# Kernel optimization log

Hardware: AMD Instinct MI355X
Metric: run time of the kernel (lower is better)

Reference implementation:

```python
import jax, jax.numpy as jnp
import numpy as np

B, S, D = 4, 2048, 1024
H = 16
HD = D // H  # 64


def setup_inputs() -> dict:
    key = jax.random.key(0)
    ks = jax.random.split(key, 5)
    std = 1.0 / np.sqrt(D)
    return {
        "x": jax.random.normal(ks[0], (B, S, D), dtype=jnp.float32),
        "Wq": jax.random.normal(ks[1], (D, D), dtype=jnp.float32) * std,
        "Wk": jax.random.normal(ks[2], (D, D), dtype=jnp.float32) * std,
        "Wv": jax.random.normal(ks[3], (D, D), dtype=jnp.float32) * std,
        "Wo": jax.random.normal(ks[4], (D, D), dtype=jnp.float32) * std,
        "bo": jnp.zeros((D,), dtype=jnp.float32),
    }


def reference(x, Wq, Wk, Wv, Wo, bo):
    b, n, d_in = x.shape
    q = (x @ Wq).reshape(b, n, H, HD).transpose(0, 2, 1, 3)  # [b,h,n,hd]
    k = (x @ Wk).reshape(b, n, H, HD).transpose(0, 2, 1, 3)
    v = (x @ Wv).reshape(b, n, H, HD).transpose(0, 2, 1, 3)
    scores = jnp.einsum("bhqd,bhkd->bhqk", q, k)  # full NxN, as in original
    causal = jnp.tril(jnp.ones((n, n), dtype=bool))  # True = keep
    scores = jnp.where(causal, scores, -jnp.inf)
    attn = jax.nn.softmax(scores / np.sqrt(HD), axis=-1)
    # dropout p=0.0 -> identity
    ctx = jnp.einsum("bhqk,bhkd->bqhd", attn, v).reshape(b, n, H * HD)
    return ctx @ Wo + bo
```

## Files before the change

### kernel.cpp

```cpp
#include <hip/hip_runtime.h>
#include <math.h>

#define BATCH 4
#define SLEN 2048
#define DMODEL 1024
#define NH 16
#define HD 64
#define MROWS (BATCH * SLEN)
#define QK_LD 2048

typedef __attribute__((ext_vector_type(8))) short short8;
typedef __attribute__((ext_vector_type(4))) float floatx4;

#define AS1 __attribute__((address_space(1)))
#define AS3 __attribute__((address_space(3)))

__device__ inline unsigned short f2bf(float f) {
    union { float f; unsigned u; } a; a.f = f;
    unsigned r = a.u + 0x7fff + ((a.u >> 16) & 1);
    return (unsigned short)(r >> 16);
}

__device__ inline unsigned pack_bf(float lo, float hi) {
    union { float f; unsigned u; } a, b; a.f = lo; b.f = hi;
    return __builtin_amdgcn_perm(b.u + 0x8000u, a.u + 0x8000u, 0x07060302u);
}
__device__ inline unsigned pack_tr(float lo, float hi) {
    union { float f; unsigned u; } a, b; a.f = lo; b.f = hi;
    return __builtin_amdgcn_perm(b.u, a.u, 0x07060302u);
}

__global__ __launch_bounds__(256) void cvt_all(
    const float* __restrict__ x,
    const float* __restrict__ Wq, const float* __restrict__ Wk,
    const float* __restrict__ Wv, const float* __restrict__ Wo,
    short* __restrict__ xb,
    short* __restrict__ WqkT, short* __restrict__ WvT, short* __restrict__ WoT)
{
    int bid = blockIdx.x;
    if (bid < 8192) {
        int i = (bid * 256 + threadIdx.x) * 4;
        float4 v = *(const float4*)(x + i);
        unsigned short t0 = f2bf(v.x), t1 = f2bf(v.y), t2 = f2bf(v.z), t3 = f2bf(v.w);
        uint2 o;
        o.x = (unsigned)t0 | ((unsigned)t1 << 16);
        o.y = (unsigned)t2 | ((unsigned)t3 << 16);
        *(uint2*)(xb + i) = o;
    } else {
        bid -= 8192;
        int z = bid >> 10;
        int inner = bid & 1023;
        int bxi = inner & 31, byi = inner >> 5;

        const float* W; short* Wt; float sc = 1.0f;
        if (z == 0)      { W = Wq; Wt = WqkT; sc = 0.18033688011112042f; }
        else if (z == 1) { W = Wk; Wt = WqkT + (size_t)DMODEL * DMODEL; }
        else if (z == 2) { W = Wv; Wt = WvT; }
        else             { W = Wo; Wt = WoT; }

        __shared__ float t[32][33];
        int bn = bxi * 32, bk = byi * 32;
        int tx = threadIdx.x & 31, r0 = (threadIdx.x >> 5) * 4;
        #pragma unroll
        for (int i = 0; i < 4; i++)
            t[r0 + i][tx] = W[(size_t)(bk + r0 + i) * DMODEL + bn + tx];
        __syncthreads();
        #pragma unroll
        for (int i = 0; i < 4; i++)
            Wt[(size_t)(bn + r0 + i) * DMODEL + bk + tx] = (short)f2bf(t[tx][r0 + i] * sc);
    }
}

#define TM 128
#define TN 128
#define TK 32

template <int OUT_BF16>
__device__ __forceinline__ void gemm_body(
    const short* __restrict__ A,
    const short* __restrict__ Bt,
    const float* __restrict__ bias,
    void* __restrict__ Cout, int N, int K, int m0, int n0)
{
    __shared__ short As[2][TM * TK];
    __shared__ short Bs[2][TN * TK];
    int tid = threadIdx.x;
    int l = tid & 63, w = tid >> 6;
    int wm = (w >> 1) * 64, wn = (w & 1) * 64;
    int lr = l & 15, lk = (l >> 4) * 8;

    const short* asrc[2];
    const short* bsrc[2];
    #pragma unroll
    for (int r = 0; r < 2; r++) {
        int c = r * 256 + tid;
        int mm = c >> 2, kk = (c & 3) * 8;
        asrc[r] = A  + (size_t)(m0 + mm) * K + kk;
        bsrc[r] = Bt + (size_t)(n0 + mm) * K + kk;
    }

    floatx4 acc[4][4] = {};

    #pragma unroll
    for (int r = 0; r < 2; r++) {
        int c = r * 256 + tid;
        __builtin_amdgcn_global_load_lds((const AS1 void*)asrc[r],
            (AS3 void*)(&As[0][0] + c * 8), 16, 0, 0);
        __builtin_amdgcn_global_load_lds((const AS1 void*)bsrc[r],
            (AS3 void*)(&Bs[0][0] + c * 8), 16, 0, 0);
        asrc[r] += TK; bsrc[r] += TK;
    }

    int nk = K / TK;
    for (int t = 0; t < nk; t++) {
        int cur = t & 1;
        if (t + 1 < nk) {
            #pragma unroll
            for (int r = 0; r < 2; r++) {
                int c = r * 256 + tid;
                __builtin_amdgcn_global_load_lds((const AS1 void*)asrc[r],
                    (AS3 void*)(&As[cur ^ 1][0] + c * 8), 16, 0, 0);
                __builtin_amdgcn_global_load_lds((const AS1 void*)bsrc[r],
                    (AS3 void*)(&Bs[cur ^ 1][0] + c * 8), 16, 0, 0);
                asrc[r] += TK; bsrc[r] += TK;
            }
            asm volatile("s_waitcnt vmcnt(4)" ::: "memory");
        } else {
            asm volatile("s_waitcnt vmcnt(0)" ::: "memory");
        }
        __builtin_amdgcn_s_barrier();
        __builtin_amdgcn_sched_barrier(0);

        short8 af[4], bg[4];
        #pragma unroll
        for (int i = 0; i < 4; i++) {
            af[i] = *(const short8*)(&As[cur][0] + (wm + i * 16 + lr) * TK + lk);
            bg[i] = *(const short8*)(&Bs[cur][0] + (wn + i * 16 + lr) * TK + lk);
        }
        #pragma unroll
        for (int mi = 0; mi < 4; mi++)
            #pragma unroll
            for (int ni = 0; ni < 4; ni++)
                acc[mi][ni] = __builtin_amdgcn_mfma_f32_16x16x32_bf16(
                    af[mi], bg[ni], acc[mi][ni], 0, 0, 0);

        __builtin_amdgcn_sched_barrier(0);
        __builtin_amdgcn_s_barrier();
    }

    int rbase = (l >> 4) * 4, cbase = l & 15;
    if (OUT_BF16) {
        short* C = (short*)Cout;
        #pragma unroll
        for (int mi = 0; mi < 4; mi++)
            #pragma unroll
            for (int r = 0; r < 4; r++) {
                int row = m0 + wm + mi * 16 + rbase + r;
                #pragma unroll
                for (int ni = 0; ni < 4; ni++) {
                    int col = n0 + wn + ni * 16 + cbase;
                    C[(size_t)row * N + col] = (short)f2bf(acc[mi][ni][r]);
                }
            }
    } else {
        float* C = (float*)Cout;
        #pragma unroll
        for (int mi = 0; mi < 4; mi++)
            #pragma unroll
            for (int r = 0; r < 4; r++) {
                int row = m0 + wm + mi * 16 + rbase + r;
                #pragma unroll
                for (int ni = 0; ni < 4; ni++) {
                    int col = n0 + wn + ni * 16 + cbase;
                    C[(size_t)row * N + col] = acc[mi][ni][r] + bias[col];
                }
            }
    }
}

template <int OUT_BF16>
__global__ __launch_bounds__(256) void mfma_gemm(
    const short* __restrict__ A, const short* __restrict__ Bt,
    const float* __restrict__ bias, void* __restrict__ Cout,
    int M, int N, int K)
{
    int m0 = blockIdx.y * TM, n0 = blockIdx.x * TN;
    gemm_body<OUT_BF16>(A, Bt, bias, Cout, N, K, m0, n0);
}

__global__ __launch_bounds__(256) void qkv_gemm(
    const short* __restrict__ xb, const short* __restrict__ WqkT,
    const short* __restrict__ WvT, short* __restrict__ QKb,
    short* __restrict__ VtT)
{
    const short* A; const short* Bt; short* C; int N, m0, n0;
    int bid = blockIdx.x;
    if (bid < 1024) {
        A = xb; Bt = WqkT; C = QKb; N = 2048;
        m0 = (bid >> 4) * TM; n0 = (bid & 15) * TN;
    } else {
        int r = bid - 1024;
        A = WvT; Bt = xb; C = VtT; N = MROWS;
        m0 = (r >> 6) * TM; n0 = (r & 63) * TN;
    }
    gemm_body<1>(A, Bt, nullptr, C, N, DMODEL, m0, n0);
}

#define PSTR 72

__global__ __launch_bounds__(256, 4) void fa_mfma(
    const short* __restrict__ QK, const short* __restrict__ VtT,
    short* __restrict__ ctx)
{
    __shared__ __align__(16) short Ks[2][64][32];
    __shared__ __align__(16) short Vs[2][64][32];
    __shared__ __align__(16) short Ps[4][16][PSTR];

    int tid = threadIdx.x;
    int l = tid & 63, w = tid >> 6;
    int lr = l & 15, lg = l >> 4;
    int bh = blockIdx.x;
    int b = bh >> 4, h = bh & 15;
    int qt = 31 - blockIdx.y;
    int q0 = qt * 64;

    const short* Qbase = QK + (size_t)b * SLEN * QK_LD + h * HD;
    const short* Kbase = Qbase + 1024;
    const short* Vbase = VtT + (size_t)h * HD * MROWS + b * SLEN;

    int xoff = (lg ^ ((lr >> 1) & 3)) * 8;

    short8 ones;
    #pragma unroll
    for (int j = 0; j < 8; j++) ones[j] = (short)0x3F80;

    int qrow = q0 + w * 16 + lr;

    short8 qf[2];
    #pragma unroll
    for (int kk = 0; kk < 2; kk++)
        qf[kk] = *(const short8*)(Qbase + (size_t)qrow * QK_LD + kk * 32 + lg * 8);

    const short* ksrc[2];
    const short* vsrc[2];
    #pragma unroll
    for (int r2 = 0; r2 < 2; r2++) {
        int cc = r2 * 256 + tid;
        int kh = cc >> 8, rr = (cc >> 2) & 63;
        int q = (cc & 3) ^ ((rr >> 1) & 3);
        ksrc[r2] = Kbase + (size_t)rr * QK_LD + kh * 32 + q * 8;
        vsrc[r2] = Vbase + (size_t)rr * MROWS + kh * 32 + q * 8;
    }

    floatx4 O[4] = {};
    floatx4 accL = {};

    for (int kt = 0; kt <= qt; kt++) {
        int k0 = kt * 64;
        __syncthreads();
        #pragma unroll
        for (int r2 = 0; r2 < 2; r2++) {
            int cc = r2 * 256 + tid;
            __builtin_amdgcn_global_load_lds(
                (const AS1 void*)ksrc[r2],
                (AS3 void*)(&Ks[0][0][0] + cc * 8), 16, 0, 0);
            __builtin_amdgcn_global_load_lds(
                (const AS1 void*)vsrc[r2],
                (AS3 void*)(&Vs[0][0][0] + cc * 8), 16, 0, 0);
            ksrc[r2] += (size_t)64 * QK_LD;
            vsrc[r2] += 64;
        }
        __syncthreads();

        floatx4 s4[4] = {};
        #pragma unroll
        for (int kk = 0; kk < 2; kk++)
            #pragma unroll
            for (int t = 0; t < 4; t++) {
                short8 kf = *(const short8*)(&Ks[kk][t * 16 + lr][xoff]);
                s4[t] = __builtin_amdgcn_mfma_f32_16x16x32_bf16(kf, qf[kk], s4[t], 0, 0, 0);
            }

        if (kt == qt) {
            #pragma unroll
            for (int t = 0; t < 4; t++)
                #pragma unroll
                for (int r = 0; r < 4; r++)
                    if (k0 + t * 16 + lg * 4 + r > qrow) s4[t][r] = -INFINITY;
        }

        #pragma unroll
        for (int t = 0; t < 4; t++) {
            float p0 = __builtin_amdgcn_exp2f(s4[t][0]);
            float p1 = __builtin_amdgcn_exp2f(s4[t][1]);
            float p2 = __builtin_amdgcn_exp2f(s4[t][2]);
            float p3 = __builtin_amdgcn_exp2f(s4[t][3]);
            uint2 pk;
            pk.x = pack_tr(p0, p1);
            pk.y = pack_tr(p2, p3);
            *(uint2*)(&Ps[w][lr][t * 16 + lg * 4]) = pk;
        }

        #pragma unroll
        for (int kk = 0; kk < 2; kk++) {
            short8 pf = *(const short8*)(&Ps[w][lr][kk * 32 + lg * 8]);
            accL = __builtin_amdgcn_mfma_f32_16x16x32_bf16(ones, pf, accL, 0, 0, 0);
            #pragma unroll
            for (int dt = 0; dt < 4; dt++) {
                short8 vf = *(const short8*)(&Vs[kk][dt * 16 + lr][xoff]);
                O[dt] = __builtin_amdgcn_mfma_f32_16x16x32_bf16(vf, pf, O[dt], 0, 0, 0);
            }
        }
    }

    float linv = 1.f / accL[0];
    short* crow = ctx + ((size_t)b * SLEN + qrow) * DMODEL + h * HD;
    #pragma unroll
    for (int dt = 0; dt < 4; dt++) {
        uint2 pk;
        pk.x = pack_bf(O[dt][0] * linv, O[dt][1] * linv);
        pk.y = pack_bf(O[dt][2] * linv, O[dt][3] * linv);
        *(uint2*)(crow + dt * 16 + lg * 4) = pk;
    }
}

extern "C" void kernel_launch(void* const* d_in, const int* in_sizes, int n_in,
                              void* d_out, int out_size, void* d_ws, size_t ws_size,
                              hipStream_t stream) {
    const float* x  = (const float*)d_in[0];
    const float* Wq = (const float*)d_in[1];
    const float* Wk = (const float*)d_in[2];
    const float* Wv = (const float*)d_in[3];
    const float* Wo = (const float*)d_in[4];
    const float* bo = (const float*)d_in[5];
    float* out = (float*)d_out;

    const size_t tsz = (size_t)MROWS * DMODEL;
    const size_t wsz = (size_t)DMODEL * DMODEL;

    short* xb    = (short*)d_ws;
    short* WqkT  = xb + tsz;
    short* WvT   = WqkT + 2 * wsz;
    short* WoT   = WvT + wsz;
    short* QKb   = WoT + wsz;
    short* VtT   = QKb + 2 * tsz;
    short* Cb    = VtT + tsz;

    cvt_all<<<12288, 256, 0, stream>>>(x, Wq, Wk, Wv, Wo, xb, WqkT, WvT, WoT);

    qkv_gemm<<<1536, 256, 0, stream>>>(xb, WqkT, WvT, QKb, VtT);

    fa_mfma<<<dim3(BATCH * NH, 32), 256, 0, stream>>>(QKb, VtT, Cb);

    mfma_gemm<0><<<dim3(DMODEL / TN, MROWS / TM), 256, 0, stream>>>(
        Cb, WoT, bo, out, MROWS, DMODEL, DMODEL);
}
```

Baseline: 240.4 us.

## Replace GEMMs with 256x256 8-wave tiled kernel, swizzled LDS and XCD remap

Replaces the 128x128x32 GEMM body with a 256x256x64 tile run by 512 threads (8 waves, each computing 128x64). A/B staging loads are interleaved with the MFMA phases, the LDS columns are XOR-swizzled to avoid bank conflicts, and s_setprio is raised around the MFMA bursts. Block IDs are remapped so neighbouring tiles land on the same XCD for L2 reuse. The goal is more data reuse per byte loaded and fewer launched blocks. The cost is heavy LDS use (128KB per block) and fewer blocks: only 128 for the output projection, which may underfill the 256 CUs.

Measured after the change: 253.3 us. 1.05x slower.

```diff
diff --git a/kernel.cpp b/kernel.cpp
--- a/kernel.cpp
+++ b/kernel.cpp
@@ -71,139 +71,155 @@
     }
 }
 
-#define TM 128
-#define TN 128
-#define TK 32
+
+#define STAGE_A(buf, h, kt) do { \
+    __builtin_amdgcn_global_load_lds((const AS1 void*)(ag + (size_t)((h) * 128) * 1024 + (kt) * 64), \
+        (AS3 void*)(&As[buf][0] + (h) * 8192 + tid * 8), 16, 0, 0); \
+    __builtin_amdgcn_global_load_lds((const AS1 void*)(ag + (size_t)((h) * 128 + 64) * 1024 + (kt) * 64), \
+        (AS3 void*)(&As[buf][0] + (h) * 8192 + 4096 + tid * 8), 16, 0, 0); \
+} while (0)
+
+#define STAGE_B(buf, h, kt) do { \
+    __builtin_amdgcn_global_load_lds((const AS1 void*)(bg + (size_t)((h) * 128) * 1024 + (kt) * 64), \
+        (AS3 void*)(&Bs[buf][0] + (h) * 8192 + tid * 8), 16, 0, 0); \
+    __builtin_amdgcn_global_load_lds((const AS1 void*)(bg + (size_t)((h) * 128 + 64) * 1024 + (kt) * 64), \
+        (AS3 void*)(&Bs[buf][0] + (h) * 8192 + 4096 + tid * 8), 16, 0, 0); \
+} while (0)
 
 template <int OUT_BF16>
-__device__ __forceinline__ void gemm_body(
+__device__ __forceinline__ void gemm8_body(
     const short* __restrict__ A,
     const short* __restrict__ Bt,
     const float* __restrict__ bias,
-    void* __restrict__ Cout, int N, int K, int m0, int n0)
-{
-    __shared__ short As[2][TM * TK];
-    __shared__ short Bs[2][TN * TK];
+    void* __restrict__ Cout, int N, int m0, int n0)
+{
+    constexpr int NT = 16;
+    __shared__ __align__(16) short As[2][256 * 64];
+    __shared__ __align__(16) short Bs[2][256 * 64];
+
     int tid = threadIdx.x;
-    int l = tid & 63, w = tid >> 6;
-    int wm = (w >> 1) * 64, wn = (w & 1) * 64;
-    int lr = l & 15, lk = (l >> 4) * 8;
-
-    const short* asrc[2];
-    const short* bsrc[2];
-    #pragma unroll
-    for (int r = 0; r < 2; r++) {
-        int c = r * 256 + tid;
-        int mm = c >> 2, kk = (c & 3) * 8;
-        asrc[r] = A  + (size_t)(m0 + mm) * K + kk;
-        bsrc[r] = Bt + (size_t)(n0 + mm) * K + kk;
-    }
-
-    floatx4 acc[4][4] = {};
-
-    #pragma unroll
-    for (int r = 0; r < 2; r++) {
-        int c = r * 256 + tid;
-        __builtin_amdgcn_global_load_lds((const AS1 void*)asrc[r],
-            (AS3 void*)(&As[0][0] + c * 8), 16, 0, 0);
-        __builtin_amdgcn_global_load_lds((const AS1 void*)bsrc[r],
-            (AS3 void*)(&Bs[0][0] + c * 8), 16, 0, 0);
-        asrc[r] += TK; bsrc[r] += TK;
-    }
-
-    int nk = K / TK;
-    for (int t = 0; t < nk; t++) {
-        int cur = t & 1;
-        if (t + 1 < nk) {
-            #pragma unroll
-            for (int r = 0; r < 2; r++) {
-                int c = r * 256 + tid;
-                __builtin_amdgcn_global_load_lds((const AS1 void*)asrc[r],
-                    (AS3 void*)(&As[cur ^ 1][0] + c * 8), 16, 0, 0);
-                __builtin_amdgcn_global_load_lds((const AS1 void*)bsrc[r],
-                    (AS3 void*)(&Bs[cur ^ 1][0] + c * 8), 16, 0, 0);
-                asrc[r] += TK; bsrc[r] += TK;
-            }
-            asm volatile("s_waitcnt vmcnt(4)" ::: "memory");
-        } else {
-            asm volatile("s_waitcnt vmcnt(0)" ::: "memory");
-        }
-        __builtin_amdgcn_s_barrier();
-        __builtin_amdgcn_sched_barrier(0);
-
-        short8 af[4], bg[4];
-        #pragma unroll
-        for (int i = 0; i < 4; i++) {
-            af[i] = *(const short8*)(&As[cur][0] + (wm + i * 16 + lr) * TK + lk);
-            bg[i] = *(const short8*)(&Bs[cur][0] + (wn + i * 16 + lr) * TK + lk);
-        }
-        #pragma unroll
-        for (int mi = 0; mi < 4; mi++)
-            #pragma unroll
-            for (int ni = 0; ni < 4; ni++)
-                acc[mi][ni] = __builtin_amdgcn_mfma_f32_16x16x32_bf16(
-                    af[mi], bg[ni], acc[mi][ni], 0, 0, 0);
-
-        __builtin_amdgcn_sched_barrier(0);
-        __builtin_amdgcn_s_barrier();
-    }
-
-    int rbase = (l >> 4) * 4, cbase = l & 15;
+    int l = tid & 63, wid = tid >> 6;
+    int wm = (wid >> 2) * 128, wn = (wid & 3) * 64;
+    int lr = l & 15, lg = l >> 4;
+    int axr = ((lr >> 2) & 1) << 4;
+
+    int r_t = tid >> 3;
+    int ce  = ((tid & 7) * 8) ^ (((tid >> 5) & 1) << 4);
+    const short* ag = A  + (size_t)(m0 + r_t) * 1024 + ce;
+    const short* bg = Bt + (size_t)(n0 + r_t) * 1024 + ce;
+
+    floatx4 acc[8][4] = {};
+
+    STAGE_A(0, 0, 0); STAGE_A(0, 1, 0);
+    STAGE_B(0, 0, 0); STAGE_B(0, 1, 0);
+    STAGE_B(1, 0, 1); STAGE_B(1, 1, 1);
+    asm volatile("s_waitcnt vmcnt(4)" ::: "memory");
+    __builtin_amdgcn_s_barrier();
+
+    #pragma unroll 2
+    for (int s = 0; s < NT; s++) {
+        int buf = s & 1;
+        short8 bfr[4][2];
+        #pragma unroll
+        for (int ni = 0; ni < 4; ni++)
+            #pragma unroll
+            for (int ks = 0; ks < 2; ks++)
+                bfr[ni][ks] = *(const short8*)(
+                    &Bs[buf][(wn + ni * 16 + lr) * 64 + ((ks * 32 + lg * 8) ^ axr)]);
+
+        #pragma unroll
+        for (int p = 0; p < 4; p++) {
+            short8 afr[2][2];
+            #pragma unroll
+            for (int m2 = 0; m2 < 2; m2++)
+                #pragma unroll
+                for (int ks = 0; ks < 2; ks++)
+                    afr[m2][ks] = *(const short8*)(
+                        &As[buf][(wm + (p * 2 + m2) * 16 + lr) * 64 + ((ks * 32 + lg * 8) ^ axr)]);
+
+            if (p == 0) { if (s + 1 < NT) STAGE_A(buf ^ 1, 0, s + 1); }
+            if (p == 1) { if (s + 1 < NT) STAGE_A(buf ^ 1, 1, s + 1); }
+            if (p == 2) { if (s + 2 < NT) STAGE_B(buf, 0, s + 2); }
+            if (p == 3) {
+                if (s + 2 < NT) {
+                    STAGE_B(buf, 1, s + 2);
+                    asm volatile("s_waitcnt vmcnt(4)" ::: "memory");
+                } else {
+                    asm volatile("s_waitcnt vmcnt(0)" ::: "memory");
+                }
+            }
+            __builtin_amdgcn_s_barrier();
+            __builtin_amdgcn_s_setprio(1);
+            #pragma unroll
+            for (int ks = 0; ks < 2; ks++)
+                #pragma unroll
+                for (int m2 = 0; m2 < 2; m2++)
+                    #pragma unroll
+                    for (int ni = 0; ni < 4; ni++)
+                        acc[p * 2 + m2][ni] = __builtin_amdgcn_mfma_f32_16x16x32_bf16(
+                            afr[m2][ks], bfr[ni][ks], acc[p * 2 + m2][ni], 0, 0, 0);
+            __builtin_amdgcn_s_setprio(0);
+            __builtin_amdgcn_s_barrier();
+        }
+    }
+
+    int rb = lg * 4;
     if (OUT_BF16) {
         short* C = (short*)Cout;
         #pragma unroll
-        for (int mi = 0; mi < 4; mi++)
+        for (int mi = 0; mi < 8; mi++)
             #pragma unroll
             for (int r = 0; r < 4; r++) {
-                int row = m0 + wm + mi * 16 + rbase + r;
+                int row = m0 + wm + mi * 16 + rb + r;
                 #pragma unroll
                 for (int ni = 0; ni < 4; ni++) {
-                    int col = n0 + wn + ni * 16 + cbase;
+                    int col = n0 + wn + ni * 16 + lr;
                     C[(size_t)row * N + col] = (short)f2bf(acc[mi][ni][r]);
                 }
             }
     } else {
         float* C = (float*)Cout;
         #pragma unroll
-        for (int mi = 0; mi < 4; mi++)
+        for (int mi = 0; mi < 8; mi++)
             #pragma unroll
             for (int r = 0; r < 4; r++) {
-                int row = m0 + wm + mi * 16 + rbase + r;
+                int row = m0 + wm + mi * 16 + rb + r;
                 #pragma unroll
                 for (int ni = 0; ni < 4; ni++) {
-                    int col = n0 + wn + ni * 16 + cbase;
+                    int col = n0 + wn + ni * 16 + lr;
                     C[(size_t)row * N + col] = acc[mi][ni][r] + bias[col];
                 }
             }
     }
 }
 
-template <int OUT_BF16>
-__global__ __launch_bounds__(256) void mfma_gemm(
-    const short* __restrict__ A, const short* __restrict__ Bt,
-    const float* __restrict__ bias, void* __restrict__ Cout,
-    int M, int N, int K)
-{
-    int m0 = blockIdx.y * TM, n0 = blockIdx.x * TN;
-    gemm_body<OUT_BF16>(A, Bt, bias, Cout, N, K, m0, n0);
-}
-
-__global__ __launch_bounds__(256) void qkv_gemm(
+__global__ __launch_bounds__(512, 2) void qkv_gemm8(
     const short* __restrict__ xb, const short* __restrict__ WqkT,
     const short* __restrict__ WvT, short* __restrict__ QKb,
     short* __restrict__ VtT)
 {
+    int bid = blockIdx.x;
+    int lgid = (bid & 7) * 48 + (bid >> 3);
     const short* A; const short* Bt; short* C; int N, m0, n0;
+    if (lgid < 256) {
+        A = xb; Bt = WqkT; C = QKb; N = 2048;
+        m0 = (lgid >> 3) * 256; n0 = (lgid & 7) * 256;
+    } else {
+        int r = lgid - 256;
+        A = WvT; Bt = xb; C = VtT; N = MROWS;
+        m0 = (r >> 5) * 256; n0 = (r & 31) * 256;
+    }
+    gemm8_body<1>(A, Bt, nullptr, C, N, m0, n0);
+}
+
+__global__ __launch_bounds__(512, 2) void o_gemm8(
+    const short* __restrict__ Cb, const short* __restrict__ WoT,
+    const float* __restrict__ bo, float* __restrict__ out)
+{
     int bid = blockIdx.x;
-    if (bid < 1024) {
-        A = xb; Bt = WqkT; C = QKb; N = 2048;
-        m0 = (bid >> 4) * TM; n0 = (bid & 15) * TN;
-    } else {
-        int r = bid - 1024;
-        A = WvT; Bt = xb; C = VtT; N = MROWS;
-        m0 = (r >> 6) * TM; n0 = (r & 63) * TN;
-    }
-    gemm_body<1>(A, Bt, nullptr, C, N, DMODEL, m0, n0);
+    int lgid = (bid & 7) * 16 + (bid >> 3);
+    int m0 = (lgid >> 2) * 256, n0 = (lgid & 3) * 256;
+    gemm8_body<0>(Cb, WoT, bo, out, DMODEL, m0, n0);
 }
 
 #define PSTR 72
@@ -348,10 +364,9 @@
 
     cvt_all<<<12288, 256, 0, stream>>>(x, Wq, Wk, Wv, Wo, xb, WqkT, WvT, WoT);
 
-    qkv_gemm<<<1536, 256, 0, stream>>>(xb, WqkT, WvT, QKb, VtT);
+    qkv_gemm8<<<384, 512, 0, stream>>>(xb, WqkT, WvT, QKb, VtT);
 
     fa_mfma<<<dim3(BATCH * NH, 32), 256, 0, stream>>>(QKb, VtT, Cb);
 
-    mfma_gemm<0><<<dim3(DMODEL / TN, MROWS / TM), 256, 0, stream>>>(
-        Cb, WoT, bo, out, MROWS, DMODEL, DMODEL);
-}
+    o_gemm8<<<128, 512, 0, stream>>>(Cb, WoT, bo, out);
+}
```

## Split K and V tile loads to overlap global-to-LDS copies with compute

Applied to the files above, without the earlier changes.

Restructures the attention inner loop so the K tile for the next step loads while the PV product uses the current V, and the next V tile loads while QK^T runs on the next K. Explicit vmcnt waits and s_barriers replace the two __syncthreads, with sched_barriers pinning instruction order. This hides global-load latency behind MFMA work using the same single LDS buffers. The cost is extra barriers per iteration and fragile hand-tuned waitcnt counts, which could break if the compiler emits other vector memory ops.

Measured after the change: 242.1 us. No clear change (+0.7%).

```diff
diff --git a/kernel.cpp b/kernel.cpp
--- a/kernel.cpp
+++ b/kernel.cpp
@@ -240,6 +240,7 @@
     #pragma unroll
     for (int kk = 0; kk < 2; kk++)
         qf[kk] = *(const short8*)(Qbase + (size_t)qrow * QK_LD + kk * 32 + lg * 8);
+    __builtin_amdgcn_sched_barrier(0);
 
     const short* ksrc[2];
     const short* vsrc[2];
@@ -255,22 +256,25 @@
     floatx4 O[4] = {};
     floatx4 accL = {};
 
+    #pragma unroll
+    for (int r2 = 0; r2 < 2; r2++) {
+        __builtin_amdgcn_global_load_lds((const AS1 void*)ksrc[r2],
+            (AS3 void*)(&Ks[0][0][0] + (r2 * 256 + tid) * 8), 16, 0, 0);
+        ksrc[r2] += (size_t)64 * QK_LD;
+    }
+    __builtin_amdgcn_sched_barrier(0);
+    #pragma unroll
+    for (int r2 = 0; r2 < 2; r2++) {
+        __builtin_amdgcn_global_load_lds((const AS1 void*)vsrc[r2],
+            (AS3 void*)(&Vs[0][0][0] + (r2 * 256 + tid) * 8), 16, 0, 0);
+        vsrc[r2] += 64;
+    }
+
     for (int kt = 0; kt <= qt; kt++) {
         int k0 = kt * 64;
-        __syncthreads();
-        #pragma unroll
-        for (int r2 = 0; r2 < 2; r2++) {
-            int cc = r2 * 256 + tid;
-            __builtin_amdgcn_global_load_lds(
-                (const AS1 void*)ksrc[r2],
-                (AS3 void*)(&Ks[0][0][0] + cc * 8), 16, 0, 0);
-            __builtin_amdgcn_global_load_lds(
-                (const AS1 void*)vsrc[r2],
-                (AS3 void*)(&Vs[0][0][0] + cc * 8), 16, 0, 0);
-            ksrc[r2] += (size_t)64 * QK_LD;
-            vsrc[r2] += 64;
-        }
-        __syncthreads();
+        asm volatile("s_waitcnt vmcnt(2)" ::: "memory");
+        __builtin_amdgcn_s_barrier();
+        __builtin_amdgcn_sched_barrier(0);
 
         floatx4 s4[4] = {};
         #pragma unroll
@@ -301,6 +305,22 @@
             *(uint2*)(&Ps[w][lr][t * 16 + lg * 4]) = pk;
         }
 
+        __builtin_amdgcn_sched_barrier(0);
+        __builtin_amdgcn_s_barrier();
+        if (kt < qt) {
+            #pragma unroll
+            for (int r2 = 0; r2 < 2; r2++) {
+                __builtin_amdgcn_global_load_lds((const AS1 void*)ksrc[r2],
+                    (AS3 void*)(&Ks[0][0][0] + (r2 * 256 + tid) * 8), 16, 0, 0);
+                ksrc[r2] += (size_t)64 * QK_LD;
+            }
+            asm volatile("s_waitcnt vmcnt(2)" ::: "memory");
+        } else {
+            asm volatile("s_waitcnt vmcnt(0)" ::: "memory");
+        }
+        __builtin_amdgcn_s_barrier();
+        __builtin_amdgcn_sched_barrier(0);
+
         #pragma unroll
         for (int kk = 0; kk < 2; kk++) {
             short8 pf = *(const short8*)(&Ps[w][lr][kk * 32 + lg * 8]);
@@ -309,6 +329,17 @@
             for (int dt = 0; dt < 4; dt++) {
                 short8 vf = *(const short8*)(&Vs[kk][dt * 16 + lr][xoff]);
                 O[dt] = __builtin_amdgcn_mfma_f32_16x16x32_bf16(vf, pf, O[dt], 0, 0, 0);
+            }
+        }
+
+        __builtin_amdgcn_sched_barrier(0);
+        __builtin_amdgcn_s_barrier();
+        if (kt < qt) {
+            #pragma unroll
+            for (int r2 = 0; r2 < 2; r2++) {
+                __builtin_amdgcn_global_load_lds((const AS1 void*)vsrc[r2],
+                    (AS3 void*)(&Vs[0][0][0] + (r2 * 256 + tid) * 8), 16, 0, 0);
+                vsrc[r2] += 64;
             }
         }
     }
```

## Fuse all stages into one persistent kernel with grid barriers and atomic tile queues

Applied to the files above, without the earlier changes.

Replaces the four separate launches (convert, QKV GEMM, flash attention, output GEMM) with a single persistent kernel of 768 blocks. The stages are separated by a software grid barrier, and each stage pulls its tiles from an atomic work counter. The aim is to cut launch gaps and tail effects, and to balance the uneven causal attention tiles dynamically. In exchange it adds barrier and atomic overhead, relies on all 768 blocks being co-resident, and forces one shared-memory size and occupancy bound on every stage, which may hurt the GEMMs.

Result: slower. 665.8 us (+176.9%).

```diff
diff --git a/kernel.cpp b/kernel.cpp
--- a/kernel.cpp
+++ b/kernel.cpp
@@ -8,12 +8,37 @@
 #define HD 64
 #define MROWS (BATCH * SLEN)
 #define QK_LD 2048
+#define NBLK 768
 
 typedef __attribute__((ext_vector_type(8))) short short8;
 typedef __attribute__((ext_vector_type(4))) float floatx4;
 
 #define AS1 __attribute__((address_space(1)))
 #define AS3 __attribute__((address_space(3)))
+
+__device__ unsigned g_cnt;
+__device__ unsigned g_gen;
+__device__ int g_t1;
+__device__ int g_t2;
+__device__ int g_t3;
+
+__device__ __forceinline__ void gbar() {
+    __syncthreads();
+    if (threadIdx.x == 0) {
+        __threadfence();
+        unsigned g = __hip_atomic_load(&g_gen, __ATOMIC_RELAXED, __HIP_MEMORY_SCOPE_AGENT);
+        unsigned a = atomicAdd(&g_cnt, 1u);
+        if (a == NBLK - 1) {
+            __hip_atomic_store(&g_cnt, 0u, __ATOMIC_RELAXED, __HIP_MEMORY_SCOPE_AGENT);
+            __hip_atomic_fetch_add(&g_gen, 1u, __ATOMIC_RELEASE, __HIP_MEMORY_SCOPE_AGENT);
+        } else {
+            while (__hip_atomic_load(&g_gen, __ATOMIC_RELAXED, __HIP_MEMORY_SCOPE_AGENT) == g)
+                __builtin_amdgcn_s_sleep(2);
+        }
+        __threadfence();
+    }
+    __syncthreads();
+}
 
 __device__ inline unsigned short f2bf(float f) {
     union { float f; unsigned u; } a; a.f = f;
@@ -30,16 +55,15 @@
     return __builtin_amdgcn_perm(b.u, a.u, 0x07060302u);
 }
 
-__global__ __launch_bounds__(256) void cvt_all(
+__device__ __forceinline__ void cvt_unit(int u, int tid,
     const float* __restrict__ x,
     const float* __restrict__ Wq, const float* __restrict__ Wk,
     const float* __restrict__ Wv, const float* __restrict__ Wo,
-    short* __restrict__ xb,
-    short* __restrict__ WqkT, short* __restrict__ WvT, short* __restrict__ WoT)
+    short* __restrict__ xb, short* __restrict__ WqkT,
+    short* __restrict__ WvT, short* __restrict__ WoT, float* t )
 {
-    int bid = blockIdx.x;
-    if (bid < 8192) {
-        int i = (bid * 256 + threadIdx.x) * 4;
+    if (u < 8192) {
+        int i = (u * 256 + tid) * 4;
         float4 v = *(const float4*)(x + i);
         unsigned short t0 = f2bf(v.x), t1 = f2bf(v.y), t2 = f2bf(v.z), t3 = f2bf(v.w);
         uint2 o;
@@ -47,9 +71,9 @@
         o.y = (unsigned)t2 | ((unsigned)t3 << 16);
         *(uint2*)(xb + i) = o;
     } else {
-        bid -= 8192;
-        int z = bid >> 10;
-        int inner = bid & 1023;
+        int v = u - 8192;
+        int z = v >> 10;
+        int inner = v & 1023;
         int bxi = inner & 31, byi = inner >> 5;
 
         const float* W; short* Wt; float sc = 1.0f;
@@ -58,16 +82,16 @@
         else if (z == 2) { W = Wv; Wt = WvT; }
         else             { W = Wo; Wt = WoT; }
 
-        __shared__ float t[32][33];
         int bn = bxi * 32, bk = byi * 32;
-        int tx = threadIdx.x & 31, r0 = (threadIdx.x >> 5) * 4;
+        int tx = tid & 31, r0 = (tid >> 5) * 4;
+        __syncthreads();
         #pragma unroll
         for (int i = 0; i < 4; i++)
-            t[r0 + i][tx] = W[(size_t)(bk + r0 + i) * DMODEL + bn + tx];
+            t[(r0 + i) * 33 + tx] = W[(size_t)(bk + r0 + i) * DMODEL + bn + tx];
         __syncthreads();
         #pragma unroll
         for (int i = 0; i < 4; i++)
-            Wt[(size_t)(bn + r0 + i) * DMODEL + bk + tx] = (short)f2bf(t[tx][r0 + i] * sc);
+            Wt[(size_t)(bn + r0 + i) * DMODEL + bk + tx] = (short)f2bf(t[tx * 33 + r0 + i] * sc);
     }
 }
 
@@ -76,14 +100,14 @@
 #define TK 32
 
 template <int OUT_BF16>
-__device__ __forceinline__ void gemm_body(
+__device__ __forceinline__ void gemm_tile(
     const short* __restrict__ A,
     const short* __restrict__ Bt,
     const float* __restrict__ bias,
-    void* __restrict__ Cout, int N, int K, int m0, int n0)
+    void* __restrict__ Cout, int N, int K, int m0, int n0, short* smem)
 {
-    __shared__ short As[2][TM * TK];
-    __shared__ short Bs[2][TN * TK];
+    short* As = smem;
+    short* Bs = smem + 8192;
     int tid = threadIdx.x;
     int l = tid & 63, w = tid >> 6;
     int wm = (w >> 1) * 64, wn = (w & 1) * 64;
@@ -105,9 +129,9 @@
     for (int r = 0; r < 2; r++) {
         int c = r * 256 + tid;
         __builtin_amdgcn_global_load_lds((const AS1 void*)asrc[r],
-            (AS3 void*)(&As[0][0] + c * 8), 16, 0, 0);
+            (AS3 void*)(As + c * 8), 16, 0, 0);
         __builtin_amdgcn_global_load_lds((const AS1 void*)bsrc[r],
-            (AS3 void*)(&Bs[0][0] + c * 8), 16, 0, 0);
+            (AS3 void*)(Bs + c * 8), 16, 0, 0);
         asrc[r] += TK; bsrc[r] += TK;
     }
 
@@ -119,9 +143,9 @@
             for (int r = 0; r < 2; r++) {
                 int c = r * 256 + tid;
                 __builtin_amdgcn_global_load_lds((const AS1 void*)asrc[r],
-                    (AS3 void*)(&As[cur ^ 1][0] + c * 8), 16, 0, 0);
+                    (AS3 void*)(As + (cur ^ 1) * 4096 + c * 8), 16, 0, 0);
                 __builtin_amdgcn_global_load_lds((const AS1 void*)bsrc[r],
-                    (AS3 void*)(&Bs[cur ^ 1][0] + c * 8), 16, 0, 0);
+                    (AS3 void*)(Bs + (cur ^ 1) * 4096 + c * 8), 16, 0, 0);
                 asrc[r] += TK; bsrc[r] += TK;
             }
             asm volatile("s_waitcnt vmcnt(4)" ::: "memory");
@@ -134,8 +158,8 @@
         short8 af[4], bg[4];
         #pragma unroll
         for (int i = 0; i < 4; i++) {
-            af[i] = *(const short8*)(&As[cur][0] + (wm + i * 16 + lr) * TK + lk);
-            bg[i] = *(const short8*)(&Bs[cur][0] + (wn + i * 16 + lr) * TK + lk);
+            af[i] = *(const short8*)(As + cur * 4096 + (wm + i * 16 + lr) * TK + lk);
+            bg[i] = *(const short8*)(Bs + cur * 4096 + (wn + i * 16 + lr) * TK + lk);
         }
         #pragma unroll
         for (int mi = 0; mi < 4; mi++)
@@ -178,50 +202,18 @@
     }
 }
 
-template <int OUT_BF16>
-__global__ __launch_bounds__(256) void mfma_gemm(
-    const short* __restrict__ A, const short* __restrict__ Bt,
-    const float* __restrict__ bias, void* __restrict__ Cout,
-    int M, int N, int K)
+#define PSTR 72
+
+__device__ __forceinline__ void fa_unit(int b, int h, int qt,
+    const short* __restrict__ QK, const short* __restrict__ VtT,
+    short* __restrict__ ctx, short* smem, int tid)
 {
-    int m0 = blockIdx.y * TM, n0 = blockIdx.x * TN;
-    gemm_body<OUT_BF16>(A, Bt, bias, Cout, N, K, m0, n0);
-}
-
-__global__ __launch_bounds__(256) void qkv_gemm(
-    const short* __restrict__ xb, const short* __restrict__ WqkT,
-    const short* __restrict__ WvT, short* __restrict__ QKb,
-    short* __restrict__ VtT)
-{
-    const short* A; const short* Bt; short* C; int N, m0, n0;
-    int bid = blockIdx.x;
-    if (bid < 1024) {
-        A = xb; Bt = WqkT; C = QKb; N = 2048;
-        m0 = (bid >> 4) * TM; n0 = (bid & 15) * TN;
-    } else {
-        int r = bid - 1024;
-        A = WvT; Bt = xb; C = VtT; N = MROWS;
-        m0 = (r >> 6) * TM; n0 = (r & 63) * TN;
-    }
-    gemm_body<1>(A, Bt, nullptr, C, N, DMODEL, m0, n0);
-}
-
-#define PSTR 72
-
-__global__ __launch_bounds__(256, 4) void fa_mfma(
-    const short* __restrict__ QK, const short* __restrict__ VtT,
-    short* __restrict__ ctx)
-{
-    __shared__ __align__(16) short Ks[2][64][32];
-    __shared__ __align__(16) short Vs[2][64][32];
-    __shared__ __align__(16) short Ps[4][16][PSTR];
-
-    int tid = threadIdx.x;
+    short* Ks = smem;
+    short* Vs = smem + 4096;
+    short* Ps = smem + 8192;
+
     int l = tid & 63, w = tid >> 6;
     int lr = l & 15, lg = l >> 4;
-    int bh = blockIdx.x;
-    int b = bh >> 4, h = bh & 15;
-    int qt = 31 - blockIdx.y;
     int q0 = qt * 64;
 
     const short* Qbase = QK + (size_t)b * SLEN * QK_LD + h * HD;
@@ -261,12 +253,10 @@
         #pragma unroll
         for (int r2 = 0; r2 < 2; r2++) {
             int cc = r2 * 256 + tid;
-            __builtin_amdgcn_global_load_lds(
-                (const AS1 void*)ksrc[r2],
-                (AS3 void*)(&Ks[0][0][0] + cc * 8), 16, 0, 0);
-            __builtin_amdgcn_global_load_lds(
-                (const AS1 void*)vsrc[r2],
-                (AS3 void*)(&Vs[0][0][0] + cc * 8), 16, 0, 0);
+            __builtin_amdgcn_global_load_lds((const AS1 void*)ksrc[r2],
+                (AS3 void*)(Ks + cc * 8), 16, 0, 0);
+            __builtin_amdgcn_global_load_lds((const AS1 void*)vsrc[r2],
+                (AS3 void*)(Vs + cc * 8), 16, 0, 0);
             ksrc[r2] += (size_t)64 * QK_LD;
             vsrc[r2] += 64;
         }
@@ -277,7 +267,7 @@
         for (int kk = 0; kk < 2; kk++)
             #pragma unroll
             for (int t = 0; t < 4; t++) {
-                short8 kf = *(const short8*)(&Ks[kk][t * 16 + lr][xoff]);
+                short8 kf = *(const short8*)(Ks + kk * 2048 + (t * 16 + lr) * 32 + xoff);
                 s4[t] = __builtin_amdgcn_mfma_f32_16x16x32_bf16(kf, qf[kk], s4[t], 0, 0, 0);
             }
 
@@ -298,16 +288,16 @@
             uint2 pk;
             pk.x = pack_tr(p0, p1);
             pk.y = pack_tr(p2, p3);
-            *(uint2*)(&Ps[w][lr][t * 16 + lg * 4]) = pk;
+            *(uint2*)(Ps + (w * 16 + lr) * PSTR + t * 16 + lg * 4) = pk;
         }
 
         #pragma unroll
         for (int kk = 0; kk < 2; kk++) {
-            short8 pf = *(const short8*)(&Ps[w][lr][kk * 32 + lg * 8]);
+            short8 pf = *(const short8*)(Ps + (w * 16 + lr) * PSTR + kk * 32 + lg * 8);
             accL = __builtin_amdgcn_mfma_f32_16x16x32_bf16(ones, pf, accL, 0, 0, 0);
             #pragma unroll
             for (int dt = 0; dt < 4; dt++) {
-                short8 vf = *(const short8*)(&Vs[kk][dt * 16 + lr][xoff]);
+                short8 vf = *(const short8*)(Vs + kk * 2048 + (dt * 16 + lr) * 32 + xoff);
                 O[dt] = __builtin_amdgcn_mfma_f32_16x16x32_bf16(vf, pf, O[dt], 0, 0, 0);
             }
         }
@@ -321,6 +311,72 @@
         pk.x = pack_bf(O[dt][0] * linv, O[dt][1] * linv);
         pk.y = pack_bf(O[dt][2] * linv, O[dt][3] * linv);
         *(uint2*)(crow + dt * 16 + lg * 4) = pk;
+    }
+}
+
+__global__ __launch_bounds__(256, 4) void mega(
+    const float* __restrict__ x,
+    const float* __restrict__ Wq, const float* __restrict__ Wk,
+    const float* __restrict__ Wv, const float* __restrict__ Wo,
+    const float* __restrict__ bo,
+    short* __restrict__ xb, short* __restrict__ WqkT,
+    short* __restrict__ WvT, short* __restrict__ WoT,
+    short* __restrict__ QKb, short* __restrict__ VtT,
+    short* __restrict__ Cb, float* __restrict__ out)
+{
+    __shared__ __align__(16) short smem[16384];
+    int tid = threadIdx.x;
+    int bid = blockIdx.x;
+
+    for (int u = bid; u < 12288; u += NBLK)
+        cvt_unit(u, tid, x, Wq, Wk, Wv, Wo, xb, WqkT, WvT, WoT, (float*)smem);
+    if (bid == 0 && tid == 0) {
+        atomicExch(&g_t1, 0);
+        atomicExch(&g_t2, 0);
+        atomicExch(&g_t3, 0);
+    }
+    gbar();
+
+    for (;;) {
+        __syncthreads();
+        if (tid == 0) ((int*)smem)[0] = atomicAdd(&g_t1, 1);
+        __syncthreads();
+        int t = ((int*)smem)[0];
+        __syncthreads();
+        if (t >= 1536) break;
+        if (t < 1024)
+            gemm_tile<1>(xb, WqkT, nullptr, QKb, 2048, DMODEL,
+                         (t >> 4) * TM, (t & 15) * TN, smem);
+        else {
+            int r = t - 1024;
+            gemm_tile<1>(WvT, xb, nullptr, VtT, MROWS, DMODEL,
+                         (r >> 6) * TM, (r & 63) * TN, smem);
+        }
+    }
+    gbar();
+
+    for (;;) {
+        __syncthreads();
+        if (tid == 0) ((int*)smem)[0] = atomicAdd(&g_t2, 1);
+        __syncthreads();
+        int t = ((int*)smem)[0];
+        __syncthreads();
+        if (t >= 2048) break;
+        int qt = 31 - (t >> 6);
+        int bh = t & 63;
+        fa_unit(bh >> 4, bh & 15, qt, QKb, VtT, Cb, smem, tid);
+    }
+    gbar();
+
+    for (;;) {
+        __syncthreads();
+        if (tid == 0) ((int*)smem)[0] = atomicAdd(&g_t3, 1);
+        __syncthreads();
+        int t = ((int*)smem)[0];
+        __syncthreads();
+        if (t >= 512) break;
+        gemm_tile<0>(Cb, WoT, bo, out, DMODEL, DMODEL,
+                     (t >> 3) * TM, (t & 7) * TN, smem);
     }
 }
 
@@ -346,12 +402,6 @@
     short* VtT   = QKb + 2 * tsz;
     short* Cb    = VtT + tsz;
 
-    cvt_all<<<12288, 256, 0, stream>>>(x, Wq, Wk, Wv, Wo, xb, WqkT, WvT, WoT);
-
-    qkv_gemm<<<1536, 256, 0, stream>>>(xb, WqkT, WvT, QKb, VtT);
-
-    fa_mfma<<<dim3(BATCH * NH, 32), 256, 0, stream>>>(QKb, VtT, Cb);
-
-    mfma_gemm<0><<<dim3(DMODEL / TN, MROWS / TM), 256, 0, stream>>>(
-        Cb, WoT, bo, out, MROWS, DMODEL, DMODEL);
-}
+    mega<<<NBLK, 256, 0, stream>>>(x, Wq, Wk, Wv, Wo, bo,
+                                   xb, WqkT, WvT, WoT, QKb, VtT, Cb, out);
+}
```
